# Kernel optimization log

Measured on AMD Instinct MI355X. Metric: run time of the kernel, lower is better.

The kernel has to match this reference:

```python
import jax, jax.numpy as jnp
import numpy as np

N, R, E, DIN, DOUT = 100000, 4, 160000, 128, 128
NEG_SLOPE = 0.2


def setup_inputs() -> dict:
    key = jax.random.key(0)
    ks = jax.random.split(key, 9)
    s_in = 1.0 / np.sqrt(DIN)
    x = jax.random.normal(ks[0], (N, DIN), jnp.float32)
    edge_src = jax.random.randint(ks[1], (R, E), 0, N)
    edge_dst = jax.random.randint(ks[2], (R, E), 0, N)
    # per-relation GATConv params (num_heads=1): fc_src, fc_dst, attn_l, attn_r, bias
    W_src = jax.random.normal(ks[3], (R, DIN, DOUT), jnp.float32) * s_in
    W_dst = jax.random.normal(ks[4], (R, DIN, DOUT), jnp.float32) * s_in
    attn_l = jax.random.normal(ks[5], (R, DOUT), jnp.float32) * 0.1
    attn_r = jax.random.normal(ks[6], (R, DOUT), jnp.float32) * 0.1
    gat_bias = jax.random.normal(ks[7], (R, DOUT), jnp.float32) * 0.01
    h_bias = jnp.zeros((DOUT,), jnp.float32)
    return {"x": x, "edge_src": edge_src, "edge_dst": edge_dst,
            "W_src": W_src, "W_dst": W_dst, "attn_l": attn_l,
            "attn_r": attn_r, "gat_bias": gat_bias, "h_bias": h_bias}


def reference(x, edge_src, edge_dst, W_src, W_dst, attn_l, attn_r, gat_bias, h_bias):
    n = x.shape[0]
    r, e = edge_src.shape
    # per-relation linear projections (GATConv fc_src / fc_dst, no bias)
    hs = jnp.einsum('nd,rde->rne', x, W_src)            # [R,N,D] source messages
    hd = jnp.einsum('nd,rde->rne', x, W_dst)            # [R,N,D] dst attn features
    el = jnp.sum(hs * attn_l[:, None, :], axis=-1)      # [R,N]
    er = jnp.sum(hd * attn_r[:, None, :], axis=-1)      # [R,N]
    rid = jnp.arange(r)[:, None]                        # [R,1]
    # edge attention logits
    logits = jax.nn.leaky_relu(
        jnp.take_along_axis(el, edge_src, axis=1)
        + jnp.take_along_axis(er, edge_dst, axis=1), NEG_SLOPE)  # [R,E]
    # edge softmax grouped by (relation, dst node): flatten into R*N segments
    seg = (edge_dst + rid * n).reshape(-1)              # [R*E]
    lf = logits.reshape(-1)
    m = jax.ops.segment_max(lf, seg, num_segments=r * n)
    a = jnp.exp(lf - m[seg])
    denom = jax.ops.segment_sum(a, seg, num_segments=r * n)
    alpha = a / denom[seg]                              # segment-normalized, denom>=1 at max edge
    msg = alpha[:, None] * hs[rid, edge_src].reshape(r * e, -1)  # [R*E,D]
    agg = jax.ops.segment_sum(msg, seg, num_segments=r * n).reshape(r, n, -1)
    agg = agg + gat_bias[:, None, :]                    # GATConv bias per relation
    h = agg.sum(0) + h_bias                             # HeteroGraphConv 'sum' + h_bias
    return jax.nn.relu(h)                               # activation; dropout eval = id; mean over 1 head = squeeze
```

## Files before the change

### kernel.cpp

```cpp
#include <hip/hip_runtime.h>
#include <hip/hip_bf16.h>

#define N_NODES 100000
#define R_REL 4
#define E_EDGES 160000
#define D 128
#define NEG_SLOPE 0.2f
#define CAP 32
#define GB 391
#define SB 313

typedef unsigned short u16x8 __attribute__((ext_vector_type(8)));
typedef unsigned short u16x4 __attribute__((ext_vector_type(4)));
typedef __bf16 bf16x8v __attribute__((ext_vector_type(8)));
typedef float f32x4 __attribute__((ext_vector_type(4)));

__device__ inline unsigned short f2bf(float f) {
    unsigned u = __float_as_uint(f);
    return (unsigned short)((u + 0x7FFFu + ((u >> 16) & 1u)) >> 16);
}
__device__ inline float bf2f(unsigned short h) {
    return __uint_as_float(((unsigned)h) << 16);
}

__global__ __launch_bounds__(512) void k_prep2(const float* __restrict__ Wsrc,
        const float* __restrict__ Wdst, const float* __restrict__ al,
        const float* __restrict__ ar, const float* __restrict__ gb,
        const float* __restrict__ hb, float* __restrict__ wl,
        float* __restrict__ wr, float* __restrict__ btot,
        unsigned short* __restrict__ Wt, unsigned* __restrict__ cnt) {
    int b = blockIdx.x, t = threadIdx.x;
    if (b == 0) {
        int r = t >> 7, d = t & 127;
        const float* as = al + r * D;
        const float* ad = ar + r * D;
        const float* rs = Wsrc + (r * D + d) * D;
        const float* rd = Wdst + (r * D + d) * D;
        float s0 = 0.f, s1 = 0.f;
        for (int e = 0; e < D; e++) { s0 += rs[e] * as[e]; s1 += rd[e] * ad[e]; }
        wl[r * D + d] = s0; wr[r * D + d] = s1;
        if (t < D) {
            float bb = hb[t];
            for (int r2 = 0; r2 < R_REL; r2++) bb += gb[r2 * D + t];
            btot[t] = bb;
        }
    } else if (b <= 32) {
        int base = (b - 1) * 2048 + t;
        #pragma unroll
        for (int i = 0; i < 4; i++) {
            int idx = base + i * 512;
            int r = idx >> 14; int rem = idx & 16383; int e = rem >> 7; int k = rem & 127;
            Wt[idx] = f2bf(Wsrc[(r * D + k) * D + e]);
        }
    } else {
        int i = (b - 33) * 512 + t;
        if (i < N_NODES) cnt[i] = 0u;
    }
}

__global__ __launch_bounds__(256) void k_scores_cast(const float* __restrict__ x,
        const float* __restrict__ wl, const float* __restrict__ wr,
        unsigned short* __restrict__ xb, float* __restrict__ el, float* __restrict__ er) {
    __shared__ float swl[R_REL * D], swr[R_REL * D];
    int t = threadIdx.x;
    for (int i = t; i < R_REL * D; i += 256) { swl[i] = wl[i]; swr[i] = wr[i]; }
    __syncthreads();
    int wv = t >> 6, lane = t & 63;
    int half = lane >> 5, q = lane & 31;
    long n = (long)blockIdx.x * 8 + wv * 2 + half;
    float4 v = ((const float4*)(x + n * D))[q];
    u16x4 ov;
    ov[0] = f2bf(v.x); ov[1] = f2bf(v.y); ov[2] = f2bf(v.z); ov[3] = f2bf(v.w);
    *(u16x4*)(xb + n * D + q * 4) = ov;
    float accl[R_REL], accr[R_REL];
    #pragma unroll
    for (int r = 0; r < R_REL; r++) {
        float4 w = ((const float4*)(swl + r * D))[q];
        accl[r] = v.x * w.x + v.y * w.y + v.z * w.z + v.w * w.w;
        float4 u = ((const float4*)(swr + r * D))[q];
        accr[r] = v.x * u.x + v.y * u.y + v.z * u.z + v.w * u.w;
    }
    #pragma unroll
    for (int r = 0; r < R_REL; r++) {
        #pragma unroll
        for (int d = 16; d >= 1; d >>= 1) {
            accl[r] += __shfl_xor(accl[r], d);
            accr[r] += __shfl_xor(accr[r], d);
        }
    }
    if (q == 0) {
        #pragma unroll
        for (int r = 0; r < R_REL; r++) {
            el[r * N_NODES + n] = accl[r];
            er[r * N_NODES + n] = accr[r];
        }
    }
}

__device__ __forceinline__ void gemm_body(int bx, int r, int tid,
        const unsigned short* __restrict__ xb, const unsigned short* __restrict__ Wt,
        unsigned short* __restrict__ hs, unsigned short (*B)[D + 8]) {
    int w = tid >> 6, l = tid & 63;
    int row16 = l & 15, kgrp = l >> 4;
    int n0 = bx * 256;
    bf16x8v a[2][4];
    int nr[2];
    #pragma unroll
    for (int rf = 0; rf < 2; rf++) {
        int nrow = n0 + w * 32 + rf * 16 + row16;
        nr[rf] = nrow;
        int nc = nrow < N_NODES ? nrow : N_NODES - 1;
        #pragma unroll
        for (int kf = 0; kf < 4; kf++)
            a[rf][kf] = *(const bf16x8v*)(xb + (long)nc * D + kf * 32 + kgrp * 8);
    }
    const unsigned short* Wr = Wt + r * D * D;
    #pragma unroll
    for (int it = 0; it < 4; it++) {
        int fi = (it * 512 + tid) * 8;
        *(u16x8*)(&B[fi >> 7][fi & 127]) = *(const u16x8*)(Wr + fi);
    }
    __syncthreads();
    f32x4 acc[2][8];
    #pragma unroll
    for (int rf = 0; rf < 2; rf++)
        #pragma unroll
        for (int et = 0; et < 8; et++) {
            acc[rf][et][0] = 0.f; acc[rf][et][1] = 0.f;
            acc[rf][et][2] = 0.f; acc[rf][et][3] = 0.f;
        }
    #pragma unroll
    for (int kf = 0; kf < 4; kf++) {
        #pragma unroll
        for (int et = 0; et < 8; et++) {
            bf16x8v av = *(const bf16x8v*)(&B[et * 16 + row16][kf * 32 + kgrp * 8]);
            acc[0][et] = __builtin_amdgcn_mfma_f32_16x16x32_bf16(av, a[0][kf], acc[0][et], 0, 0, 0);
            acc[1][et] = __builtin_amdgcn_mfma_f32_16x16x32_bf16(av, a[1][kf], acc[1][et], 0, 0, 0);
        }
    }
    #pragma unroll
    for (int rf = 0; rf < 2; rf++) {
        if (nr[rf] < N_NODES) {
            unsigned short* orow = hs + ((long)r * N_NODES + nr[rf]) * D;
            #pragma unroll
            for (int et = 0; et < 8; et++) {
                u16x4 o;
                o[0] = f2bf(acc[rf][et][0]); o[1] = f2bf(acc[rf][et][1]);
                o[2] = f2bf(acc[rf][et][2]); o[3] = f2bf(acc[rf][et][3]);
                *(u16x4*)(orow + et * 16 + kgrp * 4) = o;
            }
        }
    }
}

__device__ __forceinline__ void scatter_edge(int e, int r,
        const int* __restrict__ esrc, const int* __restrict__ edst,
        const float* __restrict__ el, const float* __restrict__ er,
        unsigned* __restrict__ cnt, int2* __restrict__ eb) {
    int t = r * E_EDGES + e;
    int src = esrc[t], dst = edst[t];
    float lg = el[r * N_NODES + src] + er[r * N_NODES + dst];
    lg = lg > 0.f ? lg : NEG_SLOPE * lg;
    float p = __expf(lg);
    unsigned pos = atomicAdd(cnt + dst, 1u);
    if (pos < CAP) eb[dst * CAP + pos] = make_int2(r * N_NODES + src, __float_as_int(p));
}

__global__ __launch_bounds__(512) void k_gemm_scatter(
        const unsigned short* __restrict__ xb, const unsigned short* __restrict__ Wt,
        unsigned short* __restrict__ hs, const int* __restrict__ esrc,
        const int* __restrict__ edst, const float* __restrict__ el,
        const float* __restrict__ er, unsigned* __restrict__ cnt,
        int2* __restrict__ eb) {
    __shared__ unsigned short B[D][D + 8];
    int bx = blockIdx.x, r = blockIdx.y, tid = threadIdx.x;
    if (bx < GB) {
        gemm_body(bx, r, tid, xb, Wt, hs, B);
    } else {
        int e = (bx - GB) * 512 + tid;
        if (e < E_EDGES) scatter_edge(e, r, esrc, edst, el, er, cnt, eb);
    }
}

__global__ __launch_bounds__(512) void k_gemm(const unsigned short* __restrict__ xb,
                                              const unsigned short* __restrict__ Wt,
                                              unsigned short* __restrict__ hs) {
    __shared__ unsigned short B[D][D + 8];
    gemm_body(blockIdx.x, blockIdx.y, threadIdx.x, xb, Wt, hs, B);
}

__global__ void k_scatter(const int* __restrict__ esrc, const int* __restrict__ edst,
                          const float* __restrict__ el, const float* __restrict__ er,
                          unsigned* __restrict__ cnt, int2* __restrict__ eb) {
    int e = blockIdx.x * 256 + threadIdx.x;
    if (e >= E_EDGES) return;
    scatter_edge(e, blockIdx.y, esrc, edst, el, er, cnt, eb);
}

__global__ __launch_bounds__(256) void k_agg(const int2* __restrict__ eb,
                                             const unsigned* __restrict__ cnt,
                                             const unsigned short* __restrict__ hs,
                                             const float* __restrict__ btot,
                                             float* __restrict__ out) {
    int wv = threadIdx.x >> 6, lane = threadIdx.x & 63;
    int half = lane >> 5, l32 = lane & 31;
    int dst = blockIdx.x * 8 + wv * 2 + half;
    unsigned num = cnt[dst];
    if (num > CAP) num = CAP;
    int rowid = 0, r = 0;
    float p = 0.f;
    if (l32 < num) {
        int2 m = eb[dst * CAP + l32];
        rowid = m.x;
        p = __int_as_float(m.y);
        r = (int)((unsigned)rowid / (unsigned)N_NODES);
    }
    float denom[R_REL];
    #pragma unroll
    for (int rr = 0; rr < R_REL; rr++) {
        float v = (r == rr) ? p : 0.f;
        #pragma unroll
        for (int d = 1; d < 32; d <<= 1) v += __shfl_xor(v, d, 32);
        denom[rr] = v;
    }
    float alpha = (l32 < num) ? p / denom[r] : 0.f;
    int slot2 = l32 >> 4, c16 = lane & 15;
    float acc[8] = {0.f, 0.f, 0.f, 0.f, 0.f, 0.f, 0.f, 0.f};
    unsigned numo = __shfl_xor(num, 32);
    unsigned numMax = num > numo ? num : numo;
    unsigned iters = (numMax + 1) >> 1;
    for (unsigned i = 0; i < iters; i++) {
        unsigned q = slot2 + i * 2;
        int srcl = half * 32 + (int)q;
        int rid = __shfl(rowid, srcl);
        float al = __shfl(alpha, srcl);
        if (q < num) {
            u16x8 v = *(const u16x8*)(hs + (long)rid * D + c16 * 8);
            #pragma unroll
            for (int j = 0; j < 8; j++) acc[j] += al * bf2f(v[j]);
        }
    }
    #pragma unroll
    for (int j = 0; j < 8; j++) acc[j] += __shfl_xor(acc[j], 16);
    if (slot2 == 0) {
        const float4 b0 = *(const float4*)(btot + c16 * 8);
        const float4 b1 = *(const float4*)(btot + c16 * 8 + 4);
        float4 o0, o1;
        o0.x = acc[0] + b0.x; o0.y = acc[1] + b0.y; o0.z = acc[2] + b0.z; o0.w = acc[3] + b0.w;
        o1.x = acc[4] + b1.x; o1.y = acc[5] + b1.y; o1.z = acc[6] + b1.z; o1.w = acc[7] + b1.w;
        o0.x = o0.x > 0.f ? o0.x : 0.f; o0.y = o0.y > 0.f ? o0.y : 0.f;
        o0.z = o0.z > 0.f ? o0.z : 0.f; o0.w = o0.w > 0.f ? o0.w : 0.f;
        o1.x = o1.x > 0.f ? o1.x : 0.f; o1.y = o1.y > 0.f ? o1.y : 0.f;
        o1.z = o1.z > 0.f ? o1.z : 0.f; o1.w = o1.w > 0.f ? o1.w : 0.f;
        *(float4*)(out + (long)dst * D + c16 * 8) = o0;
        *(float4*)(out + (long)dst * D + c16 * 8 + 4) = o1;
    }
}

extern "C" void kernel_launch(void* const* d_in, const int* in_sizes, int n_in,
                              void* d_out, int out_size, void* d_ws, size_t ws_size,
                              hipStream_t stream) {
    const float* x    = (const float*)d_in[0];
    const int*   esrc = (const int*)d_in[1];
    const int*   edst = (const int*)d_in[2];
    const float* Wsrc = (const float*)d_in[3];
    const float* Wdst = (const float*)d_in[4];
    const float* al   = (const float*)d_in[5];
    const float* ar   = (const float*)d_in[6];
    const float* gb   = (const float*)d_in[7];
    const float* hb   = (const float*)d_in[8];
    float* out = (float*)d_out;

    char* ws = (char*)d_ws;
    size_t o = 0;
    auto alloc = [&](size_t bytes) -> char* {
        char* r = ws + o; o += (bytes + 255) & ~(size_t)255; return r;
    };
    unsigned short* xb  = (unsigned short*)alloc((size_t)N_NODES * D * 2);
    unsigned short* hsb = (unsigned short*)alloc((size_t)R_REL * N_NODES * D * 2);
    unsigned short* Wt  = (unsigned short*)alloc((size_t)R_REL * D * D * 2);
    float* el   = (float*)alloc((size_t)R_REL * N_NODES * 4);
    float* er   = (float*)alloc((size_t)R_REL * N_NODES * 4);
    float* wl   = (float*)alloc(R_REL * D * 4);
    float* wr   = (float*)alloc(R_REL * D * 4);
    float* btot = (float*)alloc(D * 4);
    unsigned* cnt = (unsigned*)alloc((size_t)N_NODES * 4);
    size_t base_end = o;
    size_t eb_bytes = (size_t)N_NODES * CAP * 8;
    bool fused = (base_end + eb_bytes) <= ws_size;
    int2* eb = fused ? (int2*)alloc(eb_bytes) : (int2*)xb;

    int zblocks = (N_NODES + 511) / 512;
    k_prep2<<<dim3(33 + zblocks), dim3(512), 0, stream>>>(Wsrc, Wdst, al, ar, gb, hb,
                                                          wl, wr, btot, Wt, cnt);
    k_scores_cast<<<dim3(N_NODES / 8), dim3(256), 0, stream>>>(x, wl, wr, xb, el, er);
    if (fused) {
        k_gemm_scatter<<<dim3(GB + SB, R_REL), dim3(512), 0, stream>>>(
            xb, Wt, hsb, esrc, edst, el, er, cnt, eb);
    } else {
        k_gemm<<<dim3(GB, R_REL), dim3(512), 0, stream>>>(xb, Wt, hsb);
        k_scatter<<<dim3((E_EDGES + 255) / 256, R_REL), dim3(256), 0, stream>>>(
            esrc, edst, el, er, cnt, eb);
    }
    k_agg<<<dim3(N_NODES / 8), dim3(256), 0, stream>>>(eb, cnt, hsb, btot, out);
}
```

Baseline: 156.8 us.

## Co-schedule GEMM and edge scatter waves within each fused block

The fused kernel no longer splits the grid into separate GEMM blocks and scatter blocks. Every block now runs GEMM on its first 4 waves (128 nodes) and the edge scatter on its last 4 waves (256 edges), so the MFMA work and the atomic/gather work can overlap on the same CU. The scatter waves still help load the shared W tile and then wait at the barrier, and the GEMM tile per block is halved. The atomicAdd in scatter_edge is also moved before the logit computation so its latency overlaps with the el/er loads.

```diff
diff --git a/kernel.cpp b/kernel.cpp
--- a/kernel.cpp
+++ b/kernel.cpp
@@ -7,8 +7,7 @@
 #define D 128
 #define NEG_SLOPE 0.2f
 #define CAP 32
-#define GB 391
-#define SB 313
+#define GBX 782
 
 typedef unsigned short u16x8 __attribute__((ext_vector_type(8)));
 typedef unsigned short u16x4 __attribute__((ext_vector_type(4)));
@@ -97,72 +96,16 @@
     }
 }
 
-__device__ __forceinline__ void gemm_body(int bx, int r, int tid,
-        const unsigned short* __restrict__ xb, const unsigned short* __restrict__ Wt,
-        unsigned short* __restrict__ hs, unsigned short (*B)[D + 8]) {
-    int w = tid >> 6, l = tid & 63;
-    int row16 = l & 15, kgrp = l >> 4;
-    int n0 = bx * 256;
-    bf16x8v a[2][4];
-    int nr[2];
-    #pragma unroll
-    for (int rf = 0; rf < 2; rf++) {
-        int nrow = n0 + w * 32 + rf * 16 + row16;
-        nr[rf] = nrow;
-        int nc = nrow < N_NODES ? nrow : N_NODES - 1;
-        #pragma unroll
-        for (int kf = 0; kf < 4; kf++)
-            a[rf][kf] = *(const bf16x8v*)(xb + (long)nc * D + kf * 32 + kgrp * 8);
-    }
-    const unsigned short* Wr = Wt + r * D * D;
-    #pragma unroll
-    for (int it = 0; it < 4; it++) {
-        int fi = (it * 512 + tid) * 8;
-        *(u16x8*)(&B[fi >> 7][fi & 127]) = *(const u16x8*)(Wr + fi);
-    }
-    __syncthreads();
-    f32x4 acc[2][8];
-    #pragma unroll
-    for (int rf = 0; rf < 2; rf++)
-        #pragma unroll
-        for (int et = 0; et < 8; et++) {
-            acc[rf][et][0] = 0.f; acc[rf][et][1] = 0.f;
-            acc[rf][et][2] = 0.f; acc[rf][et][3] = 0.f;
-        }
-    #pragma unroll
-    for (int kf = 0; kf < 4; kf++) {
-        #pragma unroll
-        for (int et = 0; et < 8; et++) {
-            bf16x8v av = *(const bf16x8v*)(&B[et * 16 + row16][kf * 32 + kgrp * 8]);
-            acc[0][et] = __builtin_amdgcn_mfma_f32_16x16x32_bf16(av, a[0][kf], acc[0][et], 0, 0, 0);
-            acc[1][et] = __builtin_amdgcn_mfma_f32_16x16x32_bf16(av, a[1][kf], acc[1][et], 0, 0, 0);
-        }
-    }
-    #pragma unroll
-    for (int rf = 0; rf < 2; rf++) {
-        if (nr[rf] < N_NODES) {
-            unsigned short* orow = hs + ((long)r * N_NODES + nr[rf]) * D;
-            #pragma unroll
-            for (int et = 0; et < 8; et++) {
-                u16x4 o;
-                o[0] = f2bf(acc[rf][et][0]); o[1] = f2bf(acc[rf][et][1]);
-                o[2] = f2bf(acc[rf][et][2]); o[3] = f2bf(acc[rf][et][3]);
-                *(u16x4*)(orow + et * 16 + kgrp * 4) = o;
-            }
-        }
-    }
-}
-
 __device__ __forceinline__ void scatter_edge(int e, int r,
         const int* __restrict__ esrc, const int* __restrict__ edst,
         const float* __restrict__ el, const float* __restrict__ er,
         unsigned* __restrict__ cnt, int2* __restrict__ eb) {
     int t = r * E_EDGES + e;
     int src = esrc[t], dst = edst[t];
+    unsigned pos = atomicAdd(cnt + dst, 1u);
     float lg = el[r * N_NODES + src] + er[r * N_NODES + dst];
     lg = lg > 0.f ? lg : NEG_SLOPE * lg;
     float p = __expf(lg);
-    unsigned pos = atomicAdd(cnt + dst, 1u);
     if (pos < CAP) eb[dst * CAP + pos] = make_int2(r * N_NODES + src, __float_as_int(p));
 }
 
@@ -174,24 +117,129 @@
         int2* __restrict__ eb) {
     __shared__ unsigned short B[D][D + 8];
     int bx = blockIdx.x, r = blockIdx.y, tid = threadIdx.x;
-    if (bx < GB) {
-        gemm_body(bx, r, tid, xb, Wt, hs, B);
+    int w = tid >> 6, l = tid & 63;
+    int row16 = l & 15, kgrp = l >> 4;
+    bool isGemm = (w < 4);
+    bf16x8v a[2][4];
+    int nr[2];
+    if (isGemm) {
+        int n0 = bx * 128;
+        #pragma unroll
+        for (int rf = 0; rf < 2; rf++) {
+            int nrow = n0 + w * 32 + rf * 16 + row16;
+            nr[rf] = nrow;
+            int nc = nrow < N_NODES ? nrow : N_NODES - 1;
+            #pragma unroll
+            for (int kf = 0; kf < 4; kf++)
+                a[rf][kf] = *(const bf16x8v*)(xb + (long)nc * D + kf * 32 + kgrp * 8);
+        }
+    }
+    const unsigned short* Wr = Wt + r * D * D;
+    #pragma unroll
+    for (int it = 0; it < 4; it++) {
+        int fi = (it * 512 + tid) * 8;
+        *(u16x8*)(&B[fi >> 7][fi & 127]) = *(const u16x8*)(Wr + fi);
+    }
+    __syncthreads();
+    if (isGemm) {
+        f32x4 acc[2][8];
+        #pragma unroll
+        for (int rf = 0; rf < 2; rf++)
+            #pragma unroll
+            for (int et = 0; et < 8; et++) {
+                acc[rf][et][0] = 0.f; acc[rf][et][1] = 0.f;
+                acc[rf][et][2] = 0.f; acc[rf][et][3] = 0.f;
+            }
+        #pragma unroll
+        for (int kf = 0; kf < 4; kf++) {
+            #pragma unroll
+            for (int et = 0; et < 8; et++) {
+                bf16x8v av = *(const bf16x8v*)(&B[et * 16 + row16][kf * 32 + kgrp * 8]);
+                acc[0][et] = __builtin_amdgcn_mfma_f32_16x16x32_bf16(av, a[0][kf], acc[0][et], 0, 0, 0);
+                acc[1][et] = __builtin_amdgcn_mfma_f32_16x16x32_bf16(av, a[1][kf], acc[1][et], 0, 0, 0);
+            }
+        }
+        #pragma unroll
+        for (int rf = 0; rf < 2; rf++) {
+            if (nr[rf] < N_NODES) {
+                unsigned short* orow = hs + ((long)r * N_NODES + nr[rf]) * D;
+                #pragma unroll
+                for (int et = 0; et < 8; et++) {
+                    u16x4 o;
+                    o[0] = f2bf(acc[rf][et][0]); o[1] = f2bf(acc[rf][et][1]);
+                    o[2] = f2bf(acc[rf][et][2]); o[3] = f2bf(acc[rf][et][3]);
+                    *(u16x4*)(orow + et * 16 + kgrp * 4) = o;
+                }
+            }
+        }
     } else {
-        int e = (bx - GB) * 512 + tid;
+        int e = bx * 256 + (tid - 256);
         if (e < E_EDGES) scatter_edge(e, r, esrc, edst, el, er, cnt, eb);
     }
 }
 
-__global__ __launch_bounds__(512) void k_gemm(const unsigned short* __restrict__ xb,
-                                              const unsigned short* __restrict__ Wt,
-                                              unsigned short* __restrict__ hs) {
+__global__ __launch_bounds__(512) void k_gemm_fb(const unsigned short* __restrict__ xb,
+                                                 const unsigned short* __restrict__ Wt,
+                                                 unsigned short* __restrict__ hs) {
     __shared__ unsigned short B[D][D + 8];
-    gemm_body(blockIdx.x, blockIdx.y, threadIdx.x, xb, Wt, hs, B);
-}
-
-__global__ void k_scatter(const int* __restrict__ esrc, const int* __restrict__ edst,
-                          const float* __restrict__ el, const float* __restrict__ er,
-                          unsigned* __restrict__ cnt, int2* __restrict__ eb) {
+    int tid = threadIdx.x;
+    int w = tid >> 6, l = tid & 63;
+    int row16 = l & 15, kgrp = l >> 4;
+    int r = blockIdx.y;
+    int n0 = blockIdx.x * 256;
+    bf16x8v a[2][4];
+    int nr[2];
+    #pragma unroll
+    for (int rf = 0; rf < 2; rf++) {
+        int nrow = n0 + w * 32 + rf * 16 + row16;
+        nr[rf] = nrow;
+        int nc = nrow < N_NODES ? nrow : N_NODES - 1;
+        #pragma unroll
+        for (int kf = 0; kf < 4; kf++)
+            a[rf][kf] = *(const bf16x8v*)(xb + (long)nc * D + kf * 32 + kgrp * 8);
+    }
+    const unsigned short* Wr = Wt + r * D * D;
+    #pragma unroll
+    for (int it = 0; it < 4; it++) {
+        int fi = (it * 512 + tid) * 8;
+        *(u16x8*)(&B[fi >> 7][fi & 127]) = *(const u16x8*)(Wr + fi);
+    }
+    __syncthreads();
+    f32x4 acc[2][8];
+    #pragma unroll
+    for (int rf = 0; rf < 2; rf++)
+        #pragma unroll
+        for (int et = 0; et < 8; et++) {
+            acc[rf][et][0] = 0.f; acc[rf][et][1] = 0.f;
+            acc[rf][et][2] = 0.f; acc[rf][et][3] = 0.f;
+        }
+    #pragma unroll
+    for (int kf = 0; kf < 4; kf++) {
+        #pragma unroll
+        for (int et = 0; et < 8; et++) {
+            bf16x8v av = *(const bf16x8v*)(&B[et * 16 + row16][kf * 32 + kgrp * 8]);
+            acc[0][et] = __builtin_amdgcn_mfma_f32_16x16x32_bf16(av, a[0][kf], acc[0][et], 0, 0, 0);
+            acc[1][et] = __builtin_amdgcn_mfma_f32_16x16x32_bf16(av, a[1][kf], acc[1][et], 0, 0, 0);
+        }
+    }
+    #pragma unroll
+    for (int rf = 0; rf < 2; rf++) {
+        if (nr[rf] < N_NODES) {
+            unsigned short* orow = hs + ((long)r * N_NODES + nr[rf]) * D;
+            #pragma unroll
+            for (int et = 0; et < 8; et++) {
+                u16x4 o;
+                o[0] = f2bf(acc[rf][et][0]); o[1] = f2bf(acc[rf][et][1]);
+                o[2] = f2bf(acc[rf][et][2]); o[3] = f2bf(acc[rf][et][3]);
+                *(u16x4*)(orow + et * 16 + kgrp * 4) = o;
+            }
+        }
+    }
+}
+
+__global__ void k_scatter_fb(const int* __restrict__ esrc, const int* __restrict__ edst,
+                             const float* __restrict__ el, const float* __restrict__ er,
+                             unsigned* __restrict__ cnt, int2* __restrict__ eb) {
     int e = blockIdx.x * 256 + threadIdx.x;
     if (e >= E_EDGES) return;
     scatter_edge(e, blockIdx.y, esrc, edst, el, er, cnt, eb);
@@ -295,11 +343,11 @@
                                                           wl, wr, btot, Wt, cnt);
     k_scores_cast<<<dim3(N_NODES / 8), dim3(256), 0, stream>>>(x, wl, wr, xb, el, er);
     if (fused) {
-        k_gemm_scatter<<<dim3(GB + SB, R_REL), dim3(512), 0, stream>>>(
+        k_gemm_scatter<<<dim3(GBX, R_REL), dim3(512), 0, stream>>>(
             xb, Wt, hsb, esrc, edst, el, er, cnt, eb);
     } else {
-        k_gemm<<<dim3(GB, R_REL), dim3(512), 0, stream>>>(xb, Wt, hsb);
-        k_scatter<<<dim3((E_EDGES + 255) / 256, R_REL), dim3(256), 0, stream>>>(
+        k_gemm_fb<<<dim3((N_NODES + 255) / 256, R_REL), dim3(512), 0, stream>>>(xb, Wt, hsb);
+        k_scatter_fb<<<dim3((E_EDGES + 255) / 256, R_REL), dim3(256), 0, stream>>>(
             esrc, edst, el, er, cnt, eb);
     }
     k_agg<<<dim3(N_NODES / 8), dim3(256), 0, stream>>>(eb, cnt, hsb, btot, out);
```

New measurement: 162.6 us. +3.7%, slower.
